# Optimization experiments

Hardware: AMD Instinct MI355X
Metric: run time of the kernel (lower is better)

Reference implementation:

```python
import jax, jax.numpy as jnp
import numpy as np

B, D, K, P = 512, 2048, 128, 5

def setup_inputs() -> dict:
    key = jax.random.key(0)
    k1, k2 = jax.random.split(key)
    x = jax.random.normal(k1, (B, D), dtype=jnp.float32)
    theta = 0.05 * jax.random.normal(k2, (D, K, P), dtype=jnp.float32)
    log_weight_scale = jnp.zeros((K, P), dtype=jnp.float32)
    bias = -jnp.ones((K,), dtype=jnp.float32)  # layer inits bias to -1
    return {"x": x, "theta": theta, "log_weight_scale": log_weight_scale, "bias": bias}

def reference(x, theta, log_weight_scale, bias):
    b = x.shape[0]
    # weight-normalized kernel: [D, K, P]
    norm = jnp.sqrt(jnp.sum(theta * theta, axis=0))            # [K, P]
    kernel = theta * (jnp.exp(log_weight_scale) / norm)[None]  # [D, K, P]
    actv = jnp.einsum('bd,dkp->bkp', x, kernel)                # [B, K, P]
    # pairwise L1 over P: [B, K, B]
    diff = jnp.abs(actv[:, :, :, None] - jnp.transpose(actv, (1, 2, 0))[None])  # [B,K,P,B]
    abs_dif = jnp.sum(diff, axis=2) + 1e6 * jnp.eye(b, dtype=x.dtype)[:, None, :]
    f = jnp.sum(jnp.exp(-abs_dif), axis=2) + bias[None, :]     # [B, K]
    return jnp.concatenate([x, f], axis=1)                     # [B, D+K]
```

## Files before the change

### kernel.cpp

```cpp
#include <hip/hip_runtime.h>
#include <math.h>

#define BSZ 512
#define DD 2048
#define KK 128
#define PP 5
#define NCOL (KK * PP)
#define OUTW (DD + KK)
#define LOG2E 1.4426950408889634f

#define KSPLIT 16
#define GK (DD / KSPLIT)

typedef __attribute__((ext_vector_type(8))) short bf16x8;
typedef __attribute__((ext_vector_type(4))) float f32x4;

#define WS_NORM 0
#define WS_ACTV (WS_NORM + NCOL)
#define WS_XB (WS_ACTV + BSZ * NCOL)
#define WS_THT (WS_XB + BSZ * DD / 2)
#define WS_PART (WS_THT + NCOL * DD / 2)

__device__ inline ushort f2b(float f) {
    unsigned u = __float_as_uint(f);
    u += 0x7FFF + ((u >> 16) & 1);
    return (ushort)(u >> 16);
}

#define SWZ(r, c) ((((r) * 128) + ((c) ^ (((r) & 7) << 3))))

__global__ __launch_bounds__(256) void prep_kernel(const float* __restrict__ theta,
                                                   const float* __restrict__ x,
                                                   float* __restrict__ norm,
                                                   ushort* __restrict__ thT,
                                                   ushort* __restrict__ xb) {
    __shared__ float partial[32][8];
    __shared__ ushort sT[64][68];

    const int bid = blockIdx.x;
    const int t   = threadIdx.x;

    if (bid < 80) {
        const int c8  = bid * 8;
        const int col = c8 + (t & 7);
        const int g   = t >> 3;
        const float* p = theta + (size_t)g * NCOL + col;
        float s = 0.f;
#pragma unroll
        for (int j = 0; j < 64; ++j) {
            float v = p[(size_t)j * 32 * NCOL];
            s += v * v;
        }
        partial[g][t & 7] = s;
        __syncthreads();
        if (t < 8) {
            float acc = 0.f;
#pragma unroll
            for (int gg = 0; gg < 32; ++gg) acc += partial[gg][t];
            norm[c8 + t] = acc;
        }
    } else if (bid < 400) {
        const int tb    = bid - 80;
        const int kz    = (tb & 31) * 64;
        const int nz    = (tb >> 5) * 64;
        const int c4    = t & 15;
        const int rbase = t >> 4;
#pragma unroll
        for (int i = 0; i < 4; ++i) {
            int r = rbase + i * 16;
            float4 v = *(const float4*)&theta[(size_t)(kz + r) * NCOL + nz + c4 * 4];
            sT[c4 * 4 + 0][r] = f2b(v.x);
            sT[c4 * 4 + 1][r] = f2b(v.y);
            sT[c4 * 4 + 2][r] = f2b(v.z);
            sT[c4 * 4 + 3][r] = f2b(v.w);
        }
        __syncthreads();
#pragma unroll
        for (int i = 0; i < 2; ++i) {
            int slot = t + i * 256;
            int rr   = slot >> 3;
            int cc   = (slot & 7) * 8;
            ushort4 w0 = *(const ushort4*)&sT[rr][cc];
            ushort4 w1 = *(const ushort4*)&sT[rr][cc + 4];
            ushort* dst = &thT[(size_t)(nz + rr) * DD + kz + cc];
            *(ushort4*)&dst[0] = w0;
            *(ushort4*)&dst[4] = w1;
        }
    } else {
        const int b2 = bid - 400;
#pragma unroll
        for (int i = 0; i < 4; ++i) {
            int base = b2 * 4096 + i * 1024 + t * 4;
            float4 v = *(const float4*)&x[base];
            ushort4 w;
            w.x = f2b(v.x); w.y = f2b(v.y); w.z = f2b(v.z); w.w = f2b(v.w);
            *(ushort4*)&xb[base] = w;
        }
    }
}

__global__ __launch_bounds__(256) void gemm_kernel(const ushort* __restrict__ xb,
                                                   const ushort* __restrict__ thT,
                                                   ushort* __restrict__ parth,
                                                   const float* __restrict__ x,
                                                   float* __restrict__ out) {
    __shared__ ushort lA[64 * 128];
    __shared__ ushort lB[64 * 128];

    const int bx = blockIdx.x;
    if (bx >= 1280) {
        const int bid = bx - 1280;
        for (int i = bid * 256 + threadIdx.x; i < BSZ * (DD / 4); i += 80 * 256) {
            int r = i >> 9;
            int c = i & 511;
            float4 v = *(const float4*)&x[(size_t)r * DD + c * 4];
            *(float4*)&out[(size_t)r * OUTW + c * 4] = v;
        }
        return;
    }

    const int t    = threadIdx.x;
    const int lane = t & 63;
    const int wave = t >> 6;
    const int mt8  = bx & 7;
    const int rest = bx >> 3;
    const int bn   = (rest % 10) * 64;
    const int bm   = mt8 * 64;
    const int z    = rest / 10;
    const int kz   = z * GK;

    const ushort* gA = xb  + (size_t)bm * DD + kz;
    const ushort* gB = thT + (size_t)bn * DD + kz;

    const int srr = t >> 4;
    const int sss = t & 15;

    uint4 va[4], vb[4];
#pragma unroll
    for (int i = 0; i < 4; ++i) {
        int rr = srr + i * 16;
        va[i] = *(const uint4*)&gA[(size_t)rr * DD + sss * 8];
        vb[i] = *(const uint4*)&gB[(size_t)rr * DD + sss * 8];
    }
#pragma unroll
    for (int i = 0; i < 4; ++i) {
        int rr = srr + i * 16;
        *(uint4*)&lA[SWZ(rr, sss * 8)] = va[i];
        *(uint4*)&lB[SWZ(rr, sss * 8)] = vb[i];
    }
    __syncthreads();

    const int fr = lane & 15;
    const int g  = lane >> 4;
    const int mr = (wave >> 1) * 32 + fr;
    const int nr = (wave & 1) * 32 + fr;

    f32x4 acc[2][2] = {};
#pragma unroll
    for (int ks = 0; ks < 4; ++ks) {
        const int kc = ks * 32 + g * 8;
        bf16x8 a0 = *(const bf16x8*)&lA[SWZ(mr,      kc)];
        bf16x8 a1 = *(const bf16x8*)&lA[SWZ(mr + 16, kc)];
        bf16x8 b0 = *(const bf16x8*)&lB[SWZ(nr,      kc)];
        bf16x8 b1 = *(const bf16x8*)&lB[SWZ(nr + 16, kc)];
        acc[0][0] = __builtin_amdgcn_mfma_f32_16x16x32_bf16(a0, b0, acc[0][0], 0, 0, 0);
        acc[0][1] = __builtin_amdgcn_mfma_f32_16x16x32_bf16(a0, b1, acc[0][1], 0, 0, 0);
        acc[1][0] = __builtin_amdgcn_mfma_f32_16x16x32_bf16(a1, b0, acc[1][0], 0, 0, 0);
        acc[1][1] = __builtin_amdgcn_mfma_f32_16x16x32_bf16(a1, b1, acc[1][1], 0, 0, 0);
    }

    ushort* base = parth + (size_t)z * (BSZ * NCOL);
#pragma unroll
    for (int mt = 0; mt < 2; ++mt)
#pragma unroll
        for (int nt = 0; nt < 2; ++nt) {
            int row = bm + (wave >> 1) * 32 + mt * 16 + g * 4;
            int col = bn + (wave & 1) * 32 + nt * 16 + fr;
            ushort* dst = base + (size_t)row * NCOL + col;
#pragma unroll
            for (int reg = 0; reg < 4; ++reg)
                dst[(size_t)reg * NCOL] = f2b(acc[mt][nt][reg]);
        }
}

__global__ __launch_bounds__(256) void reduce_kernel(const ushort* __restrict__ parth,
                                                     const float* __restrict__ norm,
                                                     const float* __restrict__ lws,
                                                     float* __restrict__ actv) {
    int i = (blockIdx.x * 256 + threadIdx.x) * 2;
    float s0 = 0.f, s1 = 0.f;
#pragma unroll
    for (int q = 0; q < KSPLIT; ++q) {
        unsigned u = *(const unsigned*)&parth[(size_t)q * (BSZ * NCOL) + i];
        s0 += __uint_as_float(u << 16);
        s1 += __uint_as_float(u & 0xffff0000u);
    }
    const int col = i % NCOL;
    const float sc0 = __builtin_amdgcn_exp2f(lws[col] * LOG2E) *
                      __builtin_amdgcn_rsqf(norm[col]) * LOG2E;
    const float sc1 = __builtin_amdgcn_exp2f(lws[col + 1] * LOG2E) *
                      __builtin_amdgcn_rsqf(norm[col + 1]) * LOG2E;
    float2 o = make_float2(s0 * sc0, s1 * sc1);
    *(float2*)&actv[i] = o;
}

__global__ __launch_bounds__(256) void pairwise_kernel(const float* __restrict__ actv,
                                                       const float* __restrict__ bias,
                                                       float* __restrict__ out) {
    const int k    = blockIdx.x;
    const int rc   = blockIdx.y;
    const int tid  = threadIdx.x;
    const int lane = tid & 63;
    const int seg  = tid >> 6;

    __shared__ float sB[512][8];
    __shared__ float red[4][128];

    for (int i = tid; i < BSZ * PP; i += 256) {
        int rr = i / 5;
        int p  = i - rr * 5;
        sB[rr][p] = actv[(size_t)rr * NCOL + k * PP + p];
    }

    const int r0 = rc * 128 + lane;
    const int r1 = r0 + 64;
    float a0[PP], a1[PP];
#pragma unroll
    for (int p = 0; p < PP; ++p) {
        a0[p] = actv[(size_t)r0 * NCOL + k * PP + p];
        a1[p] = actv[(size_t)r1 * NCOL + k * PP + p];
    }
    __syncthreads();

    float acc0 = 0.f, acc1 = 0.f;
    const int j0 = seg * 128;
#pragma unroll 4
    for (int jj = 0; jj < 128; ++jj) {
        const float4 v  = *(const float4*)&sB[j0 + jj][0];
        const float  v4 = sB[j0 + jj][4];
        float s = fabsf(a0[0] - v.x) + fabsf(a0[1] - v.y) + fabsf(a0[2] - v.z) +
                  fabsf(a0[3] - v.w) + fabsf(a0[4] - v4);
        acc0 += __builtin_amdgcn_exp2f(-s);
        float t = fabsf(a1[0] - v.x) + fabsf(a1[1] - v.y) + fabsf(a1[2] - v.z) +
                  fabsf(a1[3] - v.w) + fabsf(a1[4] - v4);
        acc1 += __builtin_amdgcn_exp2f(-t);
    }
    red[seg][lane]      = acc0;
    red[seg][lane + 64] = acc1;
    __syncthreads();

    if (tid < 128) {
        float s = red[0][tid] + red[1][tid] + red[2][tid] + red[3][tid];
        out[(size_t)(rc * 128 + tid) * OUTW + DD + k] = s - 1.0f + bias[k];
    }
}

extern "C" void kernel_launch(void* const* d_in, const int* in_sizes, int n_in,
                              void* d_out, int out_size, void* d_ws, size_t ws_size,
                              hipStream_t stream) {
    const float* x     = (const float*)d_in[0];
    const float* theta = (const float*)d_in[1];
    const float* lws   = (const float*)d_in[2];
    const float* bias  = (const float*)d_in[3];
    float* out = (float*)d_out;

    float* ws     = (float*)d_ws;
    float* norm   = ws + WS_NORM;
    float* actv   = ws + WS_ACTV;
    ushort* xb    = (ushort*)(ws + WS_XB);
    ushort* thT   = (ushort*)(ws + WS_THT);
    ushort* parth = (ushort*)(ws + WS_PART);

    prep_kernel<<<656, 256, 0, stream>>>(theta, x, norm, thT, xb);
    gemm_kernel<<<1360, 256, 0, stream>>>(xb, thT, parth, x, out);
    reduce_kernel<<<640, 256, 0, stream>>>(parth, norm, lws, actv);
    pairwise_kernel<<<dim3(KK, 4), 256, 0, stream>>>(actv, bias, out);
}
```

Before: 100.7 us.

## Store actv k-major and retile pairwise kernel to 4 rows per thread

The reduce kernel now writes activations in [K][B][P] layout, so each pairwise block reads one contiguous slab instead of strided 5-float chunks spread across rows. The pairwise kernel uses 512 threads and a 128x2 grid. Each thread handles 4 query rows, taken from shared memory rather than global, over 64 candidates. The aim is to cut uncoalesced global loads and reuse each shared-memory candidate load across more rows. The cost is scattered 4-byte stores in reduce, fewer blocks (256) to fill the GPU, and a larger reduction buffer.

```diff
diff --git a/kernel.cpp b/kernel.cpp
--- a/kernel.cpp
+++ b/kernel.cpp
@@ -187,7 +187,9 @@
                                                      const float* __restrict__ norm,
                                                      const float* __restrict__ lws,
                                                      float* __restrict__ actv) {
-    int i = (blockIdx.x * 256 + threadIdx.x) * 2;
+    int i   = (blockIdx.x * 256 + threadIdx.x) * 2;
+    int b   = i / NCOL;
+    int col = i - b * NCOL;
     float s0 = 0.f, s1 = 0.f;
 #pragma unroll
     for (int q = 0; q < KSPLIT; ++q) {
@@ -195,16 +197,17 @@
         s0 += __uint_as_float(u << 16);
         s1 += __uint_as_float(u & 0xffff0000u);
     }
-    const int col = i % NCOL;
     const float sc0 = __builtin_amdgcn_exp2f(lws[col] * LOG2E) *
                       __builtin_amdgcn_rsqf(norm[col]) * LOG2E;
     const float sc1 = __builtin_amdgcn_exp2f(lws[col + 1] * LOG2E) *
                       __builtin_amdgcn_rsqf(norm[col + 1]) * LOG2E;
-    float2 o = make_float2(s0 * sc0, s1 * sc1);
-    *(float2*)&actv[i] = o;
-}
-
-__global__ __launch_bounds__(256) void pairwise_kernel(const float* __restrict__ actv,
+    int k0 = col / 5,       p0 = col - k0 * 5;
+    int k1 = (col + 1) / 5, p1 = (col + 1) - k1 * 5;
+    actv[((size_t)k0 * BSZ + b) * PP + p0] = s0 * sc0;
+    actv[((size_t)k1 * BSZ + b) * PP + p1] = s1 * sc1;
+}
+
+__global__ __launch_bounds__(512) void pairwise_kernel(const float* __restrict__ actv,
                                                        const float* __restrict__ bias,
                                                        float* __restrict__ out) {
     const int k    = blockIdx.x;
@@ -214,44 +217,46 @@
     const int seg  = tid >> 6;
 
     __shared__ float sB[512][8];
-    __shared__ float red[4][128];
-
-    for (int i = tid; i < BSZ * PP; i += 256) {
+    __shared__ float red[8][256];
+
+    const float* col = actv + (size_t)k * (BSZ * PP);
+    for (int i = tid; i < BSZ * PP; i += 512) {
         int rr = i / 5;
-        int p  = i - rr * 5;
-        sB[rr][p] = actv[(size_t)rr * NCOL + k * PP + p];
-    }
-
-    const int r0 = rc * 128 + lane;
-    const int r1 = r0 + 64;
-    float a0[PP], a1[PP];
-#pragma unroll
-    for (int p = 0; p < PP; ++p) {
-        a0[p] = actv[(size_t)r0 * NCOL + k * PP + p];
-        a1[p] = actv[(size_t)r1 * NCOL + k * PP + p];
+        sB[rr][i - rr * 5] = col[i];
     }
     __syncthreads();
 
-    float acc0 = 0.f, acc1 = 0.f;
-    const int j0 = seg * 128;
+    const int r0 = rc * 256 + lane;
+    float a[4][PP];
+#pragma unroll
+    for (int r = 0; r < 4; ++r)
+#pragma unroll
+        for (int p = 0; p < PP; ++p)
+            a[r][p] = sB[r0 + r * 64][p];
+
+    float acc[4] = {0.f, 0.f, 0.f, 0.f};
+    const int j0 = seg * 64;
 #pragma unroll 4
-    for (int jj = 0; jj < 128; ++jj) {
+    for (int jj = 0; jj < 64; ++jj) {
         const float4 v  = *(const float4*)&sB[j0 + jj][0];
         const float  v4 = sB[j0 + jj][4];
-        float s = fabsf(a0[0] - v.x) + fabsf(a0[1] - v.y) + fabsf(a0[2] - v.z) +
-                  fabsf(a0[3] - v.w) + fabsf(a0[4] - v4);
-        acc0 += __builtin_amdgcn_exp2f(-s);
-        float t = fabsf(a1[0] - v.x) + fabsf(a1[1] - v.y) + fabsf(a1[2] - v.z) +
-                  fabsf(a1[3] - v.w) + fabsf(a1[4] - v4);
-        acc1 += __builtin_amdgcn_exp2f(-t);
-    }
-    red[seg][lane]      = acc0;
-    red[seg][lane + 64] = acc1;
+#pragma unroll
+        for (int r = 0; r < 4; ++r) {
+            float s = fabsf(a[r][0] - v.x) + fabsf(a[r][1] - v.y) +
+                      fabsf(a[r][2] - v.z) + fabsf(a[r][3] - v.w) +
+                      fabsf(a[r][4] - v4);
+            acc[r] += __builtin_amdgcn_exp2f(-s);
+        }
+    }
+#pragma unroll
+    for (int r = 0; r < 4; ++r)
+        red[seg][lane + r * 64] = acc[r];
     __syncthreads();
 
-    if (tid < 128) {
-        float s = red[0][tid] + red[1][tid] + red[2][tid] + red[3][tid];
-        out[(size_t)(rc * 128 + tid) * OUTW + DD + k] = s - 1.0f + bias[k];
+    if (tid < 256) {
+        float s = red[0][tid] + red[1][tid] + red[2][tid] + red[3][tid] +
+                  red[4][tid] + red[5][tid] + red[6][tid] + red[7][tid];
+        out[(size_t)(rc * 256 + tid) * OUTW + DD + k] = s - 1.0f + bias[k];
     }
 }
 
@@ -274,5 +279,5 @@
     prep_kernel<<<656, 256, 0, stream>>>(theta, x, norm, thT, xb);
     gemm_kernel<<<1360, 256, 0, stream>>>(xb, thT, parth, x, out);
     reduce_kernel<<<640, 256, 0, stream>>>(parth, norm, lws, actv);
-    pairwise_kernel<<<dim3(KK, 4), 256, 0, stream>>>(actv, bias, out);
-}
+    pairwise_kernel<<<dim3(KK, 2), 512, 0, stream>>>(actv, bias, out);
+}
```

After: 100.1 us. No clear change (-0.6%).
